# Kernel optimization log

Measured on AMD Instinct MI355X. Metric: run time of the kernel, lower is better.

Reference implementation:

```python
import jax, jax.numpy as jnp
import numpy as np

D, L, C, CP, H, HD, QB, KB = 8, 2048, 128, 16, 4, 32, 32, 128
NQ = L // QB

def _ln(x, eps=1e-5):
    m = jnp.mean(x, axis=-1, keepdims=True)
    v = jnp.var(x, axis=-1, keepdims=True)
    return (x - m) * jax.lax.rsqrt(v + eps)

def _ada_ln(a, s, Wg, bg, Ws):
    # AF3 AdaLN: gated layernorm conditioned on s
    an = _ln(a); sn = _ln(s)
    return jax.nn.sigmoid(sn @ Wg + bg) * an + sn @ Ws

def setup_inputs() -> dict:
    key = jax.random.key(0)
    ks = jax.random.split(key, 32)
    p = lambda i, shape: jax.random.normal(ks[i], shape, dtype=jnp.float32) * 0.02
    inp = {}
    inp['A_I'] = jax.random.normal(ks[0], (D, L, C), dtype=jnp.float32)
    inp['S_I'] = jax.random.normal(ks[1], (D, L, C), dtype=jnp.float32)
    inp['Z_II'] = jax.random.normal(ks[2], (1, L, L, CP), dtype=jnp.float32)
    # static sliding-window indices: 128-key window centered on each 32-query block
    inp['indicesQ'] = jnp.arange(L, dtype=jnp.int64).reshape(NQ, QB)
    kraw = (jnp.arange(NQ) * QB - (KB - QB) // 2)[:, None] + jnp.arange(KB)[None, :]
    inp['indicesK'] = jnp.clip(kraw, 0, L - 1).astype(jnp.int64)
    inp['maskQ_float'] = jnp.zeros((NQ, QB), jnp.float32)
    inp['maskK_float'] = ((kraw < 0) | (kraw >= L)).astype(jnp.float32)
    # parameters
    inp['ada1_Wg'] = p(3, (C, C)); inp['ada1_bg'] = jnp.zeros((C,), jnp.float32); inp['ada1_Ws'] = p(4, (C, C))
    inp['Wq'] = p(5, (C, H * HD)); inp['bq'] = jnp.zeros((H * HD,), jnp.float32)
    inp['Wk'] = p(6, (C, H * HD)); inp['Wv'] = p(7, (C, H * HD))
    inp['ln0_g'] = jnp.ones((CP,), jnp.float32); inp['ln0_b'] = jnp.zeros((CP,), jnp.float32)
    inp['Wb'] = p(8, (CP, H))
    inp['Wg_attn'] = p(9, (C, H * HD))
    inp['Wa'] = p(10, (H * HD, C))
    inp['Wop'] = p(11, (C, C)); inp['bop'] = jnp.full((C,), -2.0, jnp.float32)
    inp['ada2_Wg'] = p(12, (C, C)); inp['ada2_bg'] = jnp.zeros((C,), jnp.float32); inp['ada2_Ws'] = p(13, (C, C))
    inp['W_sw'] = p(14, (C, 2 * C)); inp['W_lin'] = p(15, (C, 2 * C))
    inp['ct_Wg'] = p(16, (C, C)); inp['ct_bg'] = jnp.full((C,), -2.0, jnp.float32)
    inp['W_out2'] = p(17, (2 * C, C))
    return inp

def _forward(A_I, S_I, Z_II, indicesQ, indicesK, maskQ_float, maskK_float,
             ada1_Wg, ada1_bg, ada1_Ws, Wq, bq, Wk, Wv, ln0_g, ln0_b, Wb,
             Wg_attn, Wa, Wop, bop, ada2_Wg, ada2_bg, ada2_Ws, W_sw, W_lin,
             ct_Wg, ct_bg, W_out2):
    Dn, Lv = A_I.shape[0], A_I.shape[1]
    An = _ada_ln(A_I, S_I, ada1_Wg, ada1_bg, ada1_Ws)
    Q = (An @ Wq + bq).reshape(Dn, Lv, H, HD)
    K = (An @ Wk).reshape(Dn, Lv, H, HD)
    V = (An @ Wv).reshape(Dn, Lv, H, HD)
    B = ((_ln(Z_II) * ln0_g + ln0_b) @ Wb)[0]        # [L, L, H]
    G = jax.nn.sigmoid(An @ Wg_attn).reshape(Dn, Lv, H, HD)
    qs = Q[:, indicesQ]                              # [D, nq, qb, H, hd]
    ksub = K[:, indicesK]                            # [D, nq, kb, H, hd]
    vs = V[:, indicesK]
    attn = jnp.einsum('dnihc,dnjhc->dnijh', qs, ksub) / jnp.sqrt(jnp.float32(HD))
    bias = B[indicesQ[:, :, None], indicesK[:, None, :]]  # [nq, qb, kb, H]
    attn = attn + bias[None]
    mask = maskQ_float[None, :, :, None, None] + maskK_float[None, :, None, :, None]
    attn = attn - 1e9 * mask
    attn = jax.nn.softmax(attn, axis=-2)             # softmax over key window (j)
    af = jnp.einsum('dnijh,dnjhc->dnihc', attn, vs)
    af = af * (1.0 - maskQ_float)[None, :, :, None, None]
    af = af.reshape(Dn, -1, H, HD)[:, :Lv]
    af = (G * af).reshape(Dn, Lv, H * HD) @ Wa
    B_I = jax.nn.sigmoid(S_I @ Wop + bop) * af
    A = A_I + B_I
    an2 = _ada_ln(A, S_I, ada2_Wg, ada2_bg, ada2_Ws)
    b = jax.nn.silu(an2 @ W_sw) * (an2 @ W_lin)      # SwiGLU transition
    A = A + jax.nn.sigmoid(S_I @ ct_Wg + ct_bg) * (b @ W_out2)
    return A

def reference(A_I, S_I, Z_II, indicesQ, indicesK, maskQ_float, maskK_float,
              ada1_Wg, ada1_bg, ada1_Ws, Wq, bq, Wk, Wv, ln0_g, ln0_b, Wb,
              Wg_attn, Wa, Wop, bop, ada2_Wg, ada2_bg, ada2_Ws, W_sw, W_lin,
              ct_Wg, ct_bg, W_out2):
    return _forward(A_I, S_I, Z_II, indicesQ, indicesK, maskQ_float, maskK_float,
                    ada1_Wg, ada1_bg, ada1_Ws, Wq, bq, Wk, Wv, ln0_g, ln0_b, Wb,
                    Wg_attn, Wa, Wop, bop, ada2_Wg, ada2_bg, ada2_Ws, W_sw, W_lin,
                    ct_Wg, ct_bg, W_out2)
```

## Files before the change

### kernel.cpp

```cpp
#include <hip/hip_runtime.h>

#define DL 16384
#define LL 2048
#define NQB 64
#define QBS 32
#define KBS 128

typedef __attribute__((ext_vector_type(8))) short short8;
typedef __attribute__((ext_vector_type(4))) short short4v;
typedef __attribute__((ext_vector_type(4))) float f32x4;

__device__ __forceinline__ float sigmoidf_(float x) { return 1.f / (1.f + expf(-x)); }

__device__ __forceinline__ short f2bf(float f) {
    union { float f; unsigned u; } v; v.f = f;
    unsigned r = (v.u + 0x7FFFu + ((v.u >> 16) & 1u)) >> 16;
    return (short)r;
}
__device__ __forceinline__ float bf2f(short h) {
    union { unsigned u; float f; } v; v.u = ((unsigned)(unsigned short)h) << 16;
    return v.f;
}

#define AFRAG(buf, stride, r0, kk) (*(const short8*)&(buf)[(size_t)((r0) + cl) * (stride) + (kk) * 32 + kg * 8])
#define WFRAG(Wt, K, n0, kk) (*(const short8*)((Wt) + (size_t)((n0) + cl) * (K) + (kk) * 32 + kg * 8))
#define MFMA(acc, a, b) acc = __builtin_amdgcn_mfma_f32_16x16x32_bf16(a, b, acc, 0, 0, 0)

__global__ __launch_bounds__(256) void k_prep(
    const float* __restrict__ W0, const float* __restrict__ W1, const float* __restrict__ W2,
    const float* __restrict__ W3, const float* __restrict__ W4, const float* __restrict__ W5,
    const float* __restrict__ W6, const float* __restrict__ W7, const float* __restrict__ W8,
    const float* __restrict__ W9, const float* __restrict__ W10,
    const float* __restrict__ Wsw, const float* __restrict__ Wlin, const float* __restrict__ Wout2,
    const float* __restrict__ Z, const float* __restrict__ g16, const float* __restrict__ b16,
    const float* __restrict__ Wb,
    short* __restrict__ wout, short* __restrict__ BBt)
{
    __shared__ float sW[128 * 128];
    __shared__ float sWb[64], sg[16], sb[16];
    __shared__ short sT[4 * 4 * 128];
    const int b = blockIdx.x;
    const int tid = threadIdx.x;

    if (b < 17) {
        const float* srcs[14] = {W0,W1,W2,W3,W4,W5,W6,W7,W8,W9,W10,Wsw,Wlin,Wout2};
        const int sel[17]  = {0,1,2,3,4,5,6,7,8,9,10,11,11,12,12,13,13};
        const int soff[17] = {0,0,0,0,0,0,0,0,0,0,0, 0,128, 0,128, 0,16384};
        const int sN[17]   = {128,128,128,128,128,128,128,128,128,128,128, 256,256,256,256, 128,128};
        const int doff[17] = {0,16384,32768,49152,65536,81920,98304,114688,131072,147456,163840,
                              180224,196608, 212992,229376, 245760,245888};
        const int dK[17]   = {128,128,128,128,128,128,128,128,128,128,128, 128,128,128,128, 256,256};
        const float* src = srcs[sel[b]] + soff[b];
        const int srcN = sN[b];
        short* dst = wout + doff[b];
        const int dstK = dK[b];
        {
            const int r = tid >> 1, ch = (tid & 1) * 64;
            #pragma unroll
            for (int u = 0; u < 16; ++u) {
                float4 v = *(const float4*)(src + (size_t)r * srcN + ch + u * 4);
                *(float4*)&sW[r * 128 + ch + u * 4] = v;
            }
        }
        __syncthreads();
        {
            const int o = tid >> 1, kh = (tid & 1) * 64;
            #pragma unroll
            for (int u8 = 0; u8 < 8; ++u8) {
                short8 pk;
                #pragma unroll
                for (int e = 0; e < 8; ++e)
                    pk[e] = f2bf(sW[(kh + u8 * 8 + e) * 128 + o]);
                *(short8*)(dst + (size_t)o * dstK + kh + u8 * 8) = pk;
            }
        }
    } else {
        const int bb = b - 17;
        const int n = bb >> 3;
        const int io = (bb & 7) * 4;
        if (tid < 64) sWb[tid] = Wb[tid];
        if (tid < 16) { sg[tid] = g16[tid]; sb[tid] = b16[tid]; }
        __syncthreads();
        #pragma unroll
        for (int p = 0; p < 2; ++p) {
            int pair = tid + 256 * p;
            int il = pair >> 7, j = pair & 127;
            int i = io + il;
            int kr = n * 32 - 48 + j;
            int kc = min(max(kr, 0), LL - 1);
            const float4* z4 = (const float4*)(Z + ((long)(n * 32 + i) * LL + kc) * 16);
            float zv[16];
            #pragma unroll
            for (int w = 0; w < 4; ++w) {
                float4 v = z4[w];
                zv[w * 4 + 0] = v.x; zv[w * 4 + 1] = v.y; zv[w * 4 + 2] = v.z; zv[w * 4 + 3] = v.w;
            }
            float sm = 0.f, sq = 0.f;
            #pragma unroll
            for (int cp = 0; cp < 16; ++cp) { sm += zv[cp]; sq = fmaf(zv[cp], zv[cp], sq); }
            float m = sm * (1.f / 16.f);
            float rs = rsqrtf(sq * (1.f / 16.f) - m * m + 1e-5f);
            float b0 = 0.f, b1 = 0.f, b2 = 0.f, b3 = 0.f;
            #pragma unroll
            for (int cp = 0; cp < 16; ++cp) {
                float zn = (zv[cp] - m) * rs * sg[cp] + sb[cp];
                b0 = fmaf(zn, sWb[cp * 4 + 0], b0);
                b1 = fmaf(zn, sWb[cp * 4 + 1], b1);
                b2 = fmaf(zn, sWb[cp * 4 + 2], b2);
                b3 = fmaf(zn, sWb[cp * 4 + 3], b3);
            }
            sT[(0 * 4 + il) * 128 + j] = f2bf(b0);
            sT[(1 * 4 + il) * 128 + j] = f2bf(b1);
            sT[(2 * 4 + il) * 128 + j] = f2bf(b2);
            sT[(3 * 4 + il) * 128 + j] = f2bf(b3);
        }
        __syncthreads();
        #pragma unroll
        for (int rr = 0; rr < 2; ++rr) {
            int cid = tid + rr * 256;
            int hh = cid >> 7, j = cid & 127;
            short4v pk;
            #pragma unroll
            for (int e = 0; e < 4; ++e) pk[e] = sT[(hh * 4 + e) * 128 + j];
            *(short4v*)(BBt + (((size_t)n * 4 + hh) * 128 + j) * 32 + io) = pk;
        }
    }
}

__global__ __launch_bounds__(512) void k_adaln_qkvg(
    const float* __restrict__ A_I, const float* __restrict__ S_I,
    const short* __restrict__ Wg1t, const short* __restrict__ Ws1t,
    const short* __restrict__ Wqt, const short* __restrict__ Wkt,
    const short* __restrict__ Wvt, const short* __restrict__ Wgat,
    const float* __restrict__ bg1, const float* __restrict__ bq,
    short* __restrict__ Qo, short* __restrict__ Ko, short* __restrict__ Vo, short* __restrict__ Go)
{
    __shared__ short sAr[32 * 136];
    __shared__ short sSn[32 * 136];
    __shared__ short sAn[32 * 136];
    __shared__ float sMean[32], sRstd[32];
    const int tid = threadIdx.x;
    const int lane = tid & 63;
    const long t0 = (long)blockIdx.x * 32;

    {
        const int row = tid >> 4, seg = tid & 15;
        const float* ap = A_I + (t0 + row) * 128 + seg * 8;
        const float* sp = S_I + (t0 + row) * 128 + seg * 8;
        float av[8], sv[8];
        #pragma unroll
        for (int u = 0; u < 2; ++u) {
            float4 a4 = ((const float4*)ap)[u];
            float4 s4 = ((const float4*)sp)[u];
            av[4*u] = a4.x; av[4*u+1] = a4.y; av[4*u+2] = a4.z; av[4*u+3] = a4.w;
            sv[4*u] = s4.x; sv[4*u+1] = s4.y; sv[4*u+2] = s4.z; sv[4*u+3] = s4.w;
        }
        float am = 0.f, aq = 0.f, sm = 0.f, sq = 0.f;
        #pragma unroll
        for (int u = 0; u < 8; ++u) {
            am += av[u]; aq = fmaf(av[u], av[u], aq);
            sm += sv[u]; sq = fmaf(sv[u], sv[u], sq);
        }
        am += __shfl_xor(am, 1); am += __shfl_xor(am, 2); am += __shfl_xor(am, 4); am += __shfl_xor(am, 8);
        aq += __shfl_xor(aq, 1); aq += __shfl_xor(aq, 2); aq += __shfl_xor(aq, 4); aq += __shfl_xor(aq, 8);
        sm += __shfl_xor(sm, 1); sm += __shfl_xor(sm, 2); sm += __shfl_xor(sm, 4); sm += __shfl_xor(sm, 8);
        sq += __shfl_xor(sq, 1); sq += __shfl_xor(sq, 2); sq += __shfl_xor(sq, 4); sq += __shfl_xor(sq, 8);
        float amean = am * (1.f / 128.f);
        float arstd = rsqrtf(aq * (1.f / 128.f) - amean * amean + 1e-5f);
        float smean = sm * (1.f / 128.f);
        float srstd = rsqrtf(sq * (1.f / 128.f) - smean * smean + 1e-5f);
        if ((tid & 15) == 0) { sMean[row] = amean; sRstd[row] = arstd; }
        short8 pa, ps;
        #pragma unroll
        for (int e = 0; e < 8; ++e) {
            pa[e] = f2bf(av[e]);
            ps[e] = f2bf((sv[e] - smean) * srstd);
        }
        *(short8*)&sAr[row * 136 + seg * 8] = pa;
        *(short8*)&sSn[row * 136 + seg * 8] = ps;
    }
    __syncthreads();
    const int w = tid >> 6;
    const int n0 = w * 16;
    const int cl = lane & 15, kg = lane >> 4;
    {
        short8 wg[4], wsf[4];
        #pragma unroll
        for (int kk = 0; kk < 4; ++kk) {
            wg[kk]  = WFRAG(Wg1t, 128, n0, kk);
            wsf[kk] = WFRAG(Ws1t, 128, n0, kk);
        }
        #pragma unroll
        for (int mt = 0; mt < 2; ++mt) {
            f32x4 ag = {0.f, 0.f, 0.f, 0.f}, as = {0.f, 0.f, 0.f, 0.f};
            #pragma unroll
            for (int kk = 0; kk < 4; ++kk) {
                short8 a = AFRAG(sSn, 136, mt * 16, kk);
                MFMA(ag, a, wg[kk]);
                MFMA(as, a, wsf[kk]);
            }
            const int col = n0 + cl;
            float bgc = bg1[col];
            #pragma unroll
            for (int i = 0; i < 4; ++i) {
                int r = mt * 16 + kg * 4 + i;
                float an = (bf2f(sAr[r * 136 + col]) - sMean[r]) * sRstd[r];
                float An = sigmoidf_(ag[i] + bgc) * an + as[i];
                sAn[r * 136 + col] = f2bf(An);
            }
        }
    }
    __syncthreads();
    {
        const float SCL = 0.17677669529663687f;
        short8 af[2][4];
        #pragma unroll
        for (int mt = 0; mt < 2; ++mt)
            #pragma unroll
            for (int kk = 0; kk < 4; ++kk)
                af[mt][kk] = AFRAG(sAn, 136, mt * 16, kk);
        #pragma unroll
        for (int m = 0; m < 4; ++m) {
            const short* Wt = (m == 0) ? Wqt : (m == 1) ? Wkt : (m == 2) ? Wvt : Wgat;
            short8 wf[4];
            #pragma unroll
            for (int kk = 0; kk < 4; ++kk) wf[kk] = WFRAG(Wt, 128, n0, kk);
            #pragma unroll
            for (int mt = 0; mt < 2; ++mt) {
                f32x4 acc = {0.f, 0.f, 0.f, 0.f};
                #pragma unroll
                for (int kk = 0; kk < 4; ++kk) MFMA(acc, af[mt][kk], wf[kk]);
                const int col = n0 + cl;
                #pragma unroll
                for (int i = 0; i < 4; ++i) {
                    long t = t0 + mt * 16 + kg * 4 + i;
                    float v = acc[i];
                    if (m == 0)      Qo[t * 128 + col] = f2bf((v + bq[col]) * SCL);
                    else if (m == 1) Ko[t * 128 + col] = f2bf(v);
                    else if (m == 2) Vo[t * 128 + col] = f2bf(v);
                    else             Go[t * 128 + col] = f2bf(sigmoidf_(v));
                }
            }
        }
    }
}

__global__ __launch_bounds__(256) void k_attn(
    const short* __restrict__ Qg, const short* __restrict__ Kg, const short* __restrict__ Vg,
    const short* __restrict__ Gg, const short* __restrict__ BBt, const float* __restrict__ maskK,
    short* __restrict__ AFo)
{
    __shared__ short vts[4 * 32 * 136];
    __shared__ short Pl [4 * 32 * 136];
    const int n = blockIdx.x, d = blockIdx.y;
    const int tid = threadIdx.x;
    const int lane = tid & 63;
    const int h = tid >> 6;
    const long tb = (long)d * LL;
    const int kbase = n * 32 - 48;
    short* vtsH = vts + h * 4352;
    short* PH   = Pl  + h * 4352;
    const int cl = lane & 15, kg = lane >> 4;

    {
        const int j0 = lane * 2;
        int kc0 = min(max(kbase + j0, 0), LL - 1);
        int kc1 = min(max(kbase + j0 + 1, 0), LL - 1);
        const short8* p0 = (const short8*)(Vg + (tb + kc0) * 128 + h * 32);
        const short8* p1 = (const short8*)(Vg + (tb + kc1) * 128 + h * 32);
        short8 ev[4] = {p0[0], p0[1], p0[2], p0[3]};
        short8 ov[4] = {p1[0], p1[1], p1[2], p1[3]};
        #pragma unroll
        for (int g = 0; g < 4; ++g)
            #pragma unroll
            for (int e = 0; e < 8; ++e)
                *(unsigned*)&vtsH[(g * 8 + e) * 136 + j0] =
                    (unsigned)(unsigned short)ev[g][e] | ((unsigned)(unsigned short)ov[g][e] << 16);
    }
    __syncthreads();

    float sc[2][8][4];
    {
        short8 qf[2];
        #pragma unroll
        for (int mt = 0; mt < 2; ++mt)
            qf[mt] = *(const short8*)(Qg + (tb + n * 32 + mt * 16 + cl) * 128 + h * 32 + kg * 8);
        #pragma unroll
        for (int nt = 0; nt < 8; ++nt) {
            const int key = nt * 16 + cl;
            int kc = min(max(kbase + key, 0), LL - 1);
            short8 kf = *(const short8*)(Kg + (tb + kc) * 128 + h * 32 + kg * 8);
            float mk = maskK[n * 128 + key] * 1e9f;
            #pragma unroll
            for (int mt = 0; mt < 2; ++mt) {
                f32x4 s = {0.f, 0.f, 0.f, 0.f};
                MFMA(s, qf[mt], kf);
                short4v bfr = *(const short4v*)(BBt + (((size_t)n * 4 + h) * 128 + key) * 32 + mt * 16 + kg * 4);
                #pragma unroll
                for (int i = 0; i < 4; ++i)
                    sc[mt][nt][i] = s[i] + bf2f(bfr[i]) - mk;
            }
        }
    }
    {
        #pragma unroll
        for (int mt = 0; mt < 2; ++mt) {
            #pragma unroll
            for (int i = 0; i < 4; ++i) {
                float mx = sc[mt][0][i];
                #pragma unroll
                for (int nt = 1; nt < 8; ++nt) mx = fmaxf(mx, sc[mt][nt][i]);
                mx = fmaxf(mx, __shfl_xor(mx, 1));
                mx = fmaxf(mx, __shfl_xor(mx, 2));
                mx = fmaxf(mx, __shfl_xor(mx, 4));
                mx = fmaxf(mx, __shfl_xor(mx, 8));
                float sm = 0.f;
                #pragma unroll
                for (int nt = 0; nt < 8; ++nt) {
                    float p = __expf(sc[mt][nt][i] - mx);
                    sc[mt][nt][i] = p; sm += p;
                }
                sm += __shfl_xor(sm, 1);
                sm += __shfl_xor(sm, 2);
                sm += __shfl_xor(sm, 4);
                sm += __shfl_xor(sm, 8);
                float inv = 1.f / sm;
                const int q = mt * 16 + kg * 4 + i;
                #pragma unroll
                for (int nt = 0; nt < 8; ++nt)
                    PH[q * 136 + nt * 16 + cl] = f2bf(sc[mt][nt][i] * inv);
            }
        }
    }
    __syncthreads();
    {
        #pragma unroll
        for (int mt = 0; mt < 2; ++mt) {
            #pragma unroll
            for (int ct = 0; ct < 2; ++ct) {
                f32x4 acc = {0.f, 0.f, 0.f, 0.f};
                #pragma unroll
                for (int kk = 0; kk < 4; ++kk) {
                    short8 a = *(const short8*)&PH[(mt * 16 + cl) * 136 + kk * 32 + kg * 8];
                    short8 b = *(const short8*)&vtsH[(ct * 16 + cl) * 136 + kk * 32 + kg * 8];
                    MFMA(acc, a, b);
                }
                const int col = h * 32 + ct * 16 + cl;
                #pragma unroll
                for (int i = 0; i < 4; ++i) {
                    long t = tb + n * 32 + mt * 16 + kg * 4 + i;
                    float g = bf2f(Gg[t * 128 + col]);
                    AFo[t * 128 + col] = f2bf(g * acc[i]);
                }
            }
        }
    }
}

__global__ __launch_bounds__(512) void k_postf(
    const short* __restrict__ AF, const float* __restrict__ S_I, const float* __restrict__ A_I,
    const short* __restrict__ Wat, const short* __restrict__ Wopt, const short* __restrict__ ctWgt,
    const short* __restrict__ Wg2t, const short* __restrict__ Ws2t,
    const short* __restrict__ Wswt, const short* __restrict__ Wlint, const short* __restrict__ Wout2t,
    const float* __restrict__ bop, const float* __restrict__ ctbg, const float* __restrict__ bg2,
    float* __restrict__ Out)
{
    __shared__ __align__(16) char smem[43264];
    short* sAF  = (short*)smem;
    short* sS   = (short*)(smem + 8704);
    short* sSn  = (short*)(smem + 17408);
    float* sA   = (float*)(smem + 26112);
    float* sMean = (float*)(smem + 43008);
    float* sRstd = (float*)(smem + 43136);
    short* sAn2 = sAF;
    short* sB   = (short*)(smem + 8704);

    const int tid = threadIdx.x;
    const int lane = tid & 63;
    const long t0 = (long)blockIdx.x * 32;

    {
        const int row = tid >> 4, seg = tid & 15;
        *(short8*)&sAF[row * 136 + seg * 8] =
            *(const short8*)(AF + (t0 + row) * 128 + seg * 8);
        const float* apI = A_I + (t0 + row) * 128 + seg * 8;
        #pragma unroll
        for (int u = 0; u < 2; ++u)
            *(float4*)&sA[row * 132 + seg * 8 + u * 4] = ((const float4*)apI)[u];
        const float* sp = S_I + (t0 + row) * 128 + seg * 8;
        float sv[8];
        #pragma unroll
        for (int u = 0; u < 2; ++u) {
            float4 s4 = ((const float4*)sp)[u];
            sv[4*u] = s4.x; sv[4*u+1] = s4.y; sv[4*u+2] = s4.z; sv[4*u+3] = s4.w;
        }
        float sm = 0.f, sq = 0.f;
        #pragma unroll
        for (int u = 0; u < 8; ++u) { sm += sv[u]; sq = fmaf(sv[u], sv[u], sq); }
        sm += __shfl_xor(sm, 1); sm += __shfl_xor(sm, 2); sm += __shfl_xor(sm, 4); sm += __shfl_xor(sm, 8);
        sq += __shfl_xor(sq, 1); sq += __shfl_xor(sq, 2); sq += __shfl_xor(sq, 4); sq += __shfl_xor(sq, 8);
        float smean = sm * (1.f / 128.f);
        float srstd = rsqrtf(sq * (1.f / 128.f) - smean * smean + 1e-5f);
        short8 pr, pn;
        #pragma unroll
        for (int e = 0; e < 8; ++e) {
            float s = sv[e];
            pr[e] = f2bf(s);
            pn[e] = f2bf((s - smean) * srstd);
        }
        *(short8*)&sS [row * 136 + seg * 8] = pr;
        *(short8*)&sSn[row * 136 + seg * 8] = pn;
    }
    __syncthreads();
    const int w = tid >> 6;
    const int n0 = w * 16;
    const int cl = lane & 15, kg = lane >> 4;
    float g2s[8];

    {
        short8 wA[4], wO[4], wG[4];
        #pragma unroll
        for (int kk = 0; kk < 4; ++kk) {
            wA[kk] = WFRAG(Wat, 128, n0, kk);
            wO[kk] = WFRAG(Wopt, 128, n0, kk);
            wG[kk] = WFRAG(ctWgt, 128, n0, kk);
        }
        #pragma unroll
        for (int mt = 0; mt < 2; ++mt) {
            f32x4 aA = {0.f,0.f,0.f,0.f}, aO = {0.f,0.f,0.f,0.f}, aG = {0.f,0.f,0.f,0.f};
            #pragma unroll
            for (int kk = 0; kk < 4; ++kk) {
                short8 af = AFRAG(sAF, 136, mt * 16, kk);
                short8 sf = AFRAG(sS, 136, mt * 16, kk);
                MFMA(aA, af, wA[kk]);
                MFMA(aO, sf, wO[kk]);
                MFMA(aG, sf, wG[kk]);
            }
            const int col = n0 + cl;
            float bopc = bop[col], ctc = ctbg[col];
            #pragma unroll
            for (int i = 0; i < 4; ++i) {
                int r = mt * 16 + kg * 4 + i;
                float Aval = sA[r * 132 + col] + sigmoidf_(aO[i] + bopc) * aA[i];
                sA[r * 132 + col] = Aval;
                g2s[mt * 4 + i] = sigmoidf_(aG[i] + ctc);
            }
        }
    }
    __syncthreads();
    {
        const int row = tid >> 4, seg = tid & 15;
        float m = 0.f, q = 0.f;
        #pragma unroll
        for (int u = 0; u < 2; ++u) {
            float4 v = *(const float4*)&sA[row * 132 + seg * 8 + u * 4];
            m += v.x + v.y + v.z + v.w;
            q = fmaf(v.x, v.x, q); q = fmaf(v.y, v.y, q);
            q = fmaf(v.z, v.z, q); q = fmaf(v.w, v.w, q);
        }
        m += __shfl_xor(m, 1); m += __shfl_xor(m, 2); m += __shfl_xor(m, 4); m += __shfl_xor(m, 8);
        q += __shfl_xor(q, 1); q += __shfl_xor(q, 2); q += __shfl_xor(q, 4); q += __shfl_xor(q, 8);
        float mean = m * (1.f / 128.f);
        float rstd = rsqrtf(q * (1.f / 128.f) - mean * mean + 1e-5f);
        if ((tid & 15) == 0) { sMean[row] = mean; sRstd[row] = rstd; }
    }
    __syncthreads();
    {
        short8 wg2[4], ws2[4];
        #pragma unroll
        for (int kk = 0; kk < 4; ++kk) {
            wg2[kk] = WFRAG(Wg2t, 128, n0, kk);
            ws2[kk] = WFRAG(Ws2t, 128, n0, kk);
        }
        #pragma unroll
        for (int mt = 0; mt < 2; ++mt) {
            f32x4 ag = {0.f,0.f,0.f,0.f}, as = {0.f,0.f,0.f,0.f};
            #pragma unroll
            for (int kk = 0; kk < 4; ++kk) {
                short8 a = AFRAG(sSn, 136, mt * 16, kk);
                MFMA(ag, a, wg2[kk]);
                MFMA(as, a, ws2[kk]);
            }
            const int col = n0 + cl;
            float bg2c = bg2[col];
            #pragma unroll
            for (int i = 0; i < 4; ++i) {
                int r = mt * 16 + kg * 4 + i;
                float lnA = (sA[r * 132 + col] - sMean[r]) * sRstd[r];
                sAn2[r * 136 + col] = f2bf(sigmoidf_(ag[i] + bg2c) * lnA + as[i]);
            }
        }
    }
    __syncthreads();
    {
        short8 a2f[2][4];
        #pragma unroll
        for (int mt = 0; mt < 2; ++mt)
            #pragma unroll
            for (int kk = 0; kk < 4; ++kk)
                a2f[mt][kk] = AFRAG(sAn2, 136, mt * 16, kk);
        #pragma unroll
        for (int j = 0; j < 2; ++j) {
            const int n0b = w * 32 + j * 16;
            short8 ww[4], wl[4];
            #pragma unroll
            for (int kk = 0; kk < 4; ++kk) {
                ww[kk] = WFRAG(Wswt, 128, n0b, kk);
                wl[kk] = WFRAG(Wlint, 128, n0b, kk);
            }
            #pragma unroll
            for (int mt = 0; mt < 2; ++mt) {
                f32x4 aw = {0.f,0.f,0.f,0.f}, al = {0.f,0.f,0.f,0.f};
                #pragma unroll
                for (int kk = 0; kk < 4; ++kk) {
                    MFMA(aw, a2f[mt][kk], ww[kk]);
                    MFMA(al, a2f[mt][kk], wl[kk]);
                }
                const int col2 = n0b + cl;
                #pragma unroll
                for (int i = 0; i < 4; ++i) {
                    int r = mt * 16 + kg * 4 + i;
                    float x = aw[i];
                    float bb = (x / (1.f + expf(-x))) * al[i];
                    sB[r * 264 + col2] = f2bf(bb);
                }
            }
        }
    }
    __syncthreads();
    {
        short8 wo[8];
        #pragma unroll
        for (int kk = 0; kk < 8; ++kk) wo[kk] = WFRAG(Wout2t, 256, n0, kk);
        #pragma unroll
        for (int mt = 0; mt < 2; ++mt) {
            f32x4 acc = {0.f,0.f,0.f,0.f};
            #pragma unroll
            for (int kk = 0; kk < 8; ++kk) {
                short8 a = AFRAG(sB, 264, mt * 16, kk);
                MFMA(acc, a, wo[kk]);
            }
            const int col = n0 + cl;
            #pragma unroll
            for (int i = 0; i < 4; ++i) {
                int r = mt * 16 + kg * 4 + i;
                long t = t0 + r;
                Out[t * 128 + col] = sA[r * 132 + col] + g2s[mt * 4 + i] * acc[i];
            }
        }
    }
}

extern "C" void kernel_launch(void* const* d_in, const int* in_sizes, int n_in,
                              void* d_out, int out_size, void* d_ws, size_t ws_size,
                              hipStream_t stream)
{
    const float* A_I  = (const float*)d_in[0];
    const float* S_I  = (const float*)d_in[1];
    const float* Z    = (const float*)d_in[2];
    const float* maskK = (const float*)d_in[6];
    const float* a1Wg = (const float*)d_in[7];
    const float* a1bg = (const float*)d_in[8];
    const float* a1Ws = (const float*)d_in[9];
    const float* Wq   = (const float*)d_in[10];
    const float* bq   = (const float*)d_in[11];
    const float* Wk   = (const float*)d_in[12];
    const float* Wv   = (const float*)d_in[13];
    const float* ln0g = (const float*)d_in[14];
    const float* ln0b = (const float*)d_in[15];
    const float* Wb   = (const float*)d_in[16];
    const float* Wga  = (const float*)d_in[17];
    const float* Wa   = (const float*)d_in[18];
    const float* Wop  = (const float*)d_in[19];
    const float* bop  = (const float*)d_in[20];
    const float* a2Wg = (const float*)d_in[21];
    const float* a2bg = (const float*)d_in[22];
    const float* a2Ws = (const float*)d_in[23];
    const float* Wsw  = (const float*)d_in[24];
    const float* Wlin = (const float*)d_in[25];
    const float* ctWg = (const float*)d_in[26];
    const float* ctbg = (const float*)d_in[27];
    const float* Wout2 = (const float*)d_in[28];
    float* out = (float*)d_out;

    const size_t NTC = (size_t)DL * 128;
    short* Qb = (short*)d_ws;
    short* Kb = Qb + NTC;
    short* Vb = Kb + NTC;
    short* Gb = Vb + NTC;
    short* BBt = Gb + NTC;
    short* wbt = BBt + (size_t)NQB * 4 * 128 * 32;
    short* AFb = Qb;

    short* Wg1t = wbt + 0 * 16384;
    short* Ws1t = wbt + 1 * 16384;
    short* Wqt  = wbt + 2 * 16384;
    short* Wkt  = wbt + 3 * 16384;
    short* Wvt  = wbt + 4 * 16384;
    short* Wgat = wbt + 5 * 16384;
    short* Wat  = wbt + 6 * 16384;
    short* Wopt = wbt + 7 * 16384;
    short* ctWgt = wbt + 8 * 16384;
    short* Wg2t = wbt + 9 * 16384;
    short* Ws2t = wbt + 10 * 16384;
    short* Wswt = wbt + 180224;
    short* Wlint = wbt + 212992;
    short* Wout2t = wbt + 245760;

    k_prep<<<529, 256, 0, stream>>>(a1Wg, a1Ws, Wq, Wk, Wv, Wga, Wa, Wop, ctWg,
                                    a2Wg, a2Ws, Wsw, Wlin, Wout2,
                                    Z, ln0g, ln0b, Wb, wbt, BBt);
    k_adaln_qkvg<<<DL / 32, 512, 0, stream>>>(A_I, S_I, Wg1t, Ws1t, Wqt, Wkt, Wvt, Wgat,
                                              a1bg, bq, Qb, Kb, Vb, Gb);
    k_attn<<<dim3(NQB, 8), 256, 0, stream>>>(Qb, Kb, Vb, Gb, BBt, maskK, AFb);
    k_postf<<<DL / 32, 512, 0, stream>>>(AFb, S_I, A_I, Wat, Wopt, ctWgt, Wg2t, Ws2t,
                                         Wswt, Wlint, Wout2t, bop, ctbg, a2bg, out);
}
```

Measured before the change: 76.00 us.

## Keep softmax probabilities in registers and split attention query tiles across blocks

New measurement: 82.00 us. 1.08x slower.

```diff
diff --git a/kernel.cpp b/kernel.cpp
--- a/kernel.cpp
+++ b/kernel.cpp
@@ -17,9 +17,16 @@
     unsigned r = (v.u + 0x7FFFu + ((v.u >> 16) & 1u)) >> 16;
     return (short)r;
 }
+__device__ __forceinline__ unsigned f2bfu(float f) {
+    union { float f; unsigned u; } v; v.f = f;
+    return (v.u + 0x7FFFu + ((v.u >> 16) & 1u)) >> 16;
+}
 __device__ __forceinline__ float bf2f(short h) {
     union { unsigned u; float f; } v; v.u = ((unsigned)(unsigned short)h) << 16;
     return v.f;
+}
+__device__ __forceinline__ unsigned packbf(float a, float b) {
+    return (f2bfu(a) & 0xFFFFu) | (f2bfu(b) << 16);
 }
 
 #define AFRAG(buf, stride, r0, kk) (*(const short8*)&(buf)[(size_t)((r0) + cl) * (stride) + (kk) * 32 + kg * 8])
@@ -81,48 +88,52 @@
         if (tid < 64) sWb[tid] = Wb[tid];
         if (tid < 16) { sg[tid] = g16[tid]; sb[tid] = b16[tid]; }
         __syncthreads();
-        #pragma unroll
-        for (int p = 0; p < 2; ++p) {
-            int pair = tid + 256 * p;
-            int il = pair >> 7, j = pair & 127;
+        const int q4 = tid & 3;
+        #pragma unroll
+        for (int p = 0; p < 8; ++p) {
+            int pairIdx = p * 64 + (tid >> 2);
+            int il = pairIdx >> 7, j = pairIdx & 127;
             int i = io + il;
             int kr = n * 32 - 48 + j;
             int kc = min(max(kr, 0), LL - 1);
-            const float4* z4 = (const float4*)(Z + ((long)(n * 32 + i) * LL + kc) * 16);
-            float zv[16];
-            #pragma unroll
-            for (int w = 0; w < 4; ++w) {
-                float4 v = z4[w];
-                zv[w * 4 + 0] = v.x; zv[w * 4 + 1] = v.y; zv[w * 4 + 2] = v.z; zv[w * 4 + 3] = v.w;
-            }
-            float sm = 0.f, sq = 0.f;
-            #pragma unroll
-            for (int cp = 0; cp < 16; ++cp) { sm += zv[cp]; sq = fmaf(zv[cp], zv[cp], sq); }
+            float4 zv = *(const float4*)(Z + ((long)(n * 32 + i) * LL + kc) * 16 + q4 * 4);
+            float sm = zv.x + zv.y + zv.z + zv.w;
+            float sq = fmaf(zv.x, zv.x, fmaf(zv.y, zv.y, fmaf(zv.z, zv.z, zv.w * zv.w)));
+            sm += __shfl_xor(sm, 1); sm += __shfl_xor(sm, 2);
+            sq += __shfl_xor(sq, 1); sq += __shfl_xor(sq, 2);
             float m = sm * (1.f / 16.f);
             float rs = rsqrtf(sq * (1.f / 16.f) - m * m + 1e-5f);
+            float zn[4];
+            zn[0] = (zv.x - m) * rs * sg[q4 * 4 + 0] + sb[q4 * 4 + 0];
+            zn[1] = (zv.y - m) * rs * sg[q4 * 4 + 1] + sb[q4 * 4 + 1];
+            zn[2] = (zv.z - m) * rs * sg[q4 * 4 + 2] + sb[q4 * 4 + 2];
+            zn[3] = (zv.w - m) * rs * sg[q4 * 4 + 3] + sb[q4 * 4 + 3];
             float b0 = 0.f, b1 = 0.f, b2 = 0.f, b3 = 0.f;
             #pragma unroll
-            for (int cp = 0; cp < 16; ++cp) {
-                float zn = (zv[cp] - m) * rs * sg[cp] + sb[cp];
-                b0 = fmaf(zn, sWb[cp * 4 + 0], b0);
-                b1 = fmaf(zn, sWb[cp * 4 + 1], b1);
-                b2 = fmaf(zn, sWb[cp * 4 + 2], b2);
-                b3 = fmaf(zn, sWb[cp * 4 + 3], b3);
-            }
-            sT[(0 * 4 + il) * 128 + j] = f2bf(b0);
-            sT[(1 * 4 + il) * 128 + j] = f2bf(b1);
-            sT[(2 * 4 + il) * 128 + j] = f2bf(b2);
-            sT[(3 * 4 + il) * 128 + j] = f2bf(b3);
+            for (int e = 0; e < 4; ++e) {
+                int cp = q4 * 4 + e;
+                b0 = fmaf(zn[e], sWb[cp * 4 + 0], b0);
+                b1 = fmaf(zn[e], sWb[cp * 4 + 1], b1);
+                b2 = fmaf(zn[e], sWb[cp * 4 + 2], b2);
+                b3 = fmaf(zn[e], sWb[cp * 4 + 3], b3);
+            }
+            b0 += __shfl_xor(b0, 1); b0 += __shfl_xor(b0, 2);
+            b1 += __shfl_xor(b1, 1); b1 += __shfl_xor(b1, 2);
+            b2 += __shfl_xor(b2, 1); b2 += __shfl_xor(b2, 2);
+            b3 += __shfl_xor(b3, 1); b3 += __shfl_xor(b3, 2);
+            float vh = (q4 == 0) ? b0 : (q4 == 1) ? b1 : (q4 == 2) ? b2 : b3;
+            sT[(q4 * 4 + il) * 128 + j] = f2bf(vh);
         }
         __syncthreads();
         #pragma unroll
         for (int rr = 0; rr < 2; ++rr) {
             int cid = tid + rr * 256;
-            int hh = cid >> 7, j = cid & 127;
+            int hh = cid >> 7, r2 = cid & 127;
+            int il = r2 >> 5, jb = (r2 & 31) * 4;
             short4v pk;
             #pragma unroll
-            for (int e = 0; e < 4; ++e) pk[e] = sT[(hh * 4 + e) * 128 + j];
-            *(short4v*)(BBt + (((size_t)n * 4 + hh) * 128 + j) * 32 + io) = pk;
+            for (int e = 0; e < 4; ++e) pk[e] = sT[(hh * 4 + il) * 128 + jb + e];
+            *(short4v*)(BBt + (((size_t)n * 4 + hh) * 32 + io + il) * 128 + jb) = pk;
         }
     }
 }
@@ -251,15 +262,13 @@
     short* __restrict__ AFo)
 {
     __shared__ short vts[4 * 32 * 136];
-    __shared__ short Pl [4 * 32 * 136];
-    const int n = blockIdx.x, d = blockIdx.y;
+    const int n = blockIdx.x, d = blockIdx.y, mt = blockIdx.z;
     const int tid = threadIdx.x;
     const int lane = tid & 63;
     const int h = tid >> 6;
     const long tb = (long)d * LL;
     const int kbase = n * 32 - 48;
     short* vtsH = vts + h * 4352;
-    short* PH   = Pl  + h * 4352;
     const int cl = lane & 15, kg = lane >> 4;
 
     {
@@ -277,82 +286,83 @@
                 *(unsigned*)&vtsH[(g * 8 + e) * 136 + j0] =
                     (unsigned)(unsigned short)ev[g][e] | ((unsigned)(unsigned short)ov[g][e] << 16);
     }
-    __syncthreads();
-
-    float sc[2][8][4];
-    {
-        short8 qf[2];
-        #pragma unroll
-        for (int mt = 0; mt < 2; ++mt)
-            qf[mt] = *(const short8*)(Qg + (tb + n * 32 + mt * 16 + cl) * 128 + h * 32 + kg * 8);
+
+    float sc[8][4];
+    {
+        short8 qf = *(const short8*)(Qg + (tb + n * 32 + mt * 16 + cl) * 128 + h * 32 + kg * 8);
         #pragma unroll
         for (int nt = 0; nt < 8; ++nt) {
-            const int key = nt * 16 + cl;
-            int kc = min(max(kbase + key, 0), LL - 1);
+            int kc = min(max(kbase + nt * 16 + cl, 0), LL - 1);
             short8 kf = *(const short8*)(Kg + (tb + kc) * 128 + h * 32 + kg * 8);
-            float mk = maskK[n * 128 + key] * 1e9f;
-            #pragma unroll
-            for (int mt = 0; mt < 2; ++mt) {
-                f32x4 s = {0.f, 0.f, 0.f, 0.f};
-                MFMA(s, qf[mt], kf);
-                short4v bfr = *(const short4v*)(BBt + (((size_t)n * 4 + h) * 128 + key) * 32 + mt * 16 + kg * 4);
-                #pragma unroll
-                for (int i = 0; i < 4; ++i)
-                    sc[mt][nt][i] = s[i] + bf2f(bfr[i]) - mk;
-            }
-        }
-    }
-    {
-        #pragma unroll
-        for (int mt = 0; mt < 2; ++mt) {
+            f32x4 s = {0.f, 0.f, 0.f, 0.f};
+            MFMA(s, kf, qf);
+            float4 mk4 = *(const float4*)(maskK + n * 128 + nt * 16 + kg * 4);
+            short4v bfr = *(const short4v*)(BBt + (((size_t)n * 4 + h) * 32 + mt * 16 + cl) * 128 + nt * 16 + kg * 4);
+            #pragma unroll
+            for (int i = 0; i < 4; ++i)
+                sc[nt][i] = s[i] + bf2f(bfr[i]) - mk4[i] * 1e9f;
+        }
+    }
+    unsigned bfrag[4][4];
+    {
+        float mx = sc[0][0];
+        #pragma unroll
+        for (int nt = 0; nt < 8; ++nt)
+            #pragma unroll
+            for (int i = 0; i < 4; ++i) mx = fmaxf(mx, sc[nt][i]);
+        mx = fmaxf(mx, __shfl_xor(mx, 16));
+        mx = fmaxf(mx, __shfl_xor(mx, 32));
+        float sm = 0.f;
+        #pragma unroll
+        for (int nt = 0; nt < 8; ++nt)
             #pragma unroll
             for (int i = 0; i < 4; ++i) {
-                float mx = sc[mt][0][i];
-                #pragma unroll
-                for (int nt = 1; nt < 8; ++nt) mx = fmaxf(mx, sc[mt][nt][i]);
-                mx = fmaxf(mx, __shfl_xor(mx, 1));
-                mx = fmaxf(mx, __shfl_xor(mx, 2));
-                mx = fmaxf(mx, __shfl_xor(mx, 4));
-                mx = fmaxf(mx, __shfl_xor(mx, 8));
-                float sm = 0.f;
-                #pragma unroll
-                for (int nt = 0; nt < 8; ++nt) {
-                    float p = __expf(sc[mt][nt][i] - mx);
-                    sc[mt][nt][i] = p; sm += p;
-                }
-                sm += __shfl_xor(sm, 1);
-                sm += __shfl_xor(sm, 2);
-                sm += __shfl_xor(sm, 4);
-                sm += __shfl_xor(sm, 8);
-                float inv = 1.f / sm;
-                const int q = mt * 16 + kg * 4 + i;
-                #pragma unroll
-                for (int nt = 0; nt < 8; ++nt)
-                    PH[q * 136 + nt * 16 + cl] = f2bf(sc[mt][nt][i] * inv);
-            }
-        }
-    }
-    __syncthreads();
-    {
-        #pragma unroll
-        for (int mt = 0; mt < 2; ++mt) {
-            #pragma unroll
-            for (int ct = 0; ct < 2; ++ct) {
-                f32x4 acc = {0.f, 0.f, 0.f, 0.f};
-                #pragma unroll
-                for (int kk = 0; kk < 4; ++kk) {
-                    short8 a = *(const short8*)&PH[(mt * 16 + cl) * 136 + kk * 32 + kg * 8];
-                    short8 b = *(const short8*)&vtsH[(ct * 16 + cl) * 136 + kk * 32 + kg * 8];
-                    MFMA(acc, a, b);
-                }
-                const int col = h * 32 + ct * 16 + cl;
-                #pragma unroll
-                for (int i = 0; i < 4; ++i) {
-                    long t = tb + n * 32 + mt * 16 + kg * 4 + i;
-                    float g = bf2f(Gg[t * 128 + col]);
-                    AFo[t * 128 + col] = f2bf(g * acc[i]);
-                }
-            }
+                float p = __expf(sc[nt][i] - mx);
+                sc[nt][i] = p; sm += p;
+            }
+        sm += __shfl_xor(sm, 16);
+        sm += __shfl_xor(sm, 32);
+        float inv = 1.f / sm;
+        #pragma unroll
+        for (int c2 = 0; c2 < 4; ++c2) {
+            unsigned E0 = packbf(sc[2*c2][0] * inv, sc[2*c2][1] * inv);
+            unsigned E1 = packbf(sc[2*c2][2] * inv, sc[2*c2][3] * inv);
+            unsigned O0 = packbf(sc[2*c2+1][0] * inv, sc[2*c2+1][1] * inv);
+            unsigned O1 = packbf(sc[2*c2+1][2] * inv, sc[2*c2+1][3] * inv);
+            unsigned t0 = (kg < 2) ? O0 : E0;
+            unsigned t1 = (kg < 2) ? O1 : E1;
+            unsigned r10 = __shfl_xor((int)t0, 32);
+            unsigned r11 = __shfl_xor((int)t1, 32);
+            unsigned u0 = (kg == 0 || kg == 3) ? r10 : (kg == 1 ? E0 : O0);
+            unsigned u1 = (kg == 0 || kg == 3) ? r11 : (kg == 1 ? E1 : O1);
+            unsigned r20 = __shfl_xor((int)u0, 16);
+            unsigned r21 = __shfl_xor((int)u1, 16);
+            bfrag[c2][0] = (kg == 0) ? E0 : (kg == 2) ? r10 : r20;
+            bfrag[c2][1] = (kg == 0) ? E1 : (kg == 2) ? r11 : r21;
+            bfrag[c2][2] = (kg == 0) ? r20 : (kg == 1) ? r10 : (kg == 2) ? r20 : O0;
+            bfrag[c2][3] = (kg == 0) ? r21 : (kg == 1) ? r11 : (kg == 2) ? r21 : O1;
+        }
+    }
+    __syncthreads();
+    {
+        #pragma unroll
+        for (int ct = 0; ct < 2; ++ct) {
+            f32x4 acc = {0.f, 0.f, 0.f, 0.f};
+            #pragma unroll
+            for (int c2 = 0; c2 < 4; ++c2) {
+                short8 a = *(const short8*)&vtsH[(ct * 16 + cl) * 136 + c2 * 32 + kg * 8];
+                union { unsigned u[4]; short8 s; } bb;
+                bb.u[0] = bfrag[c2][0]; bb.u[1] = bfrag[c2][1];
+                bb.u[2] = bfrag[c2][2]; bb.u[3] = bfrag[c2][3];
+                MFMA(acc, a, bb.s);
+            }
+            long t = tb + n * 32 + mt * 16 + cl;
+            const int c0 = h * 32 + ct * 16 + kg * 4;
+            short4v g4 = *(const short4v*)(Gg + t * 128 + c0);
+            short4v o4;
+            #pragma unroll
+            for (int i = 0; i < 4; ++i) o4[i] = f2bf(bf2f(g4[i]) * acc[i]);
+            *(short4v*)(AFo + t * 128 + c0) = o4;
         }
     }
 }
@@ -589,7 +599,7 @@
     short* Vb = Kb + NTC;
     short* Gb = Vb + NTC;
     short* BBt = Gb + NTC;
-    short* wbt = BBt + (size_t)NQB * 4 * 128 * 32;
+    short* wbt = BBt + (size_t)NQB * 4 * 32 * 128;
     short* AFb = Qb;
 
     short* Wg1t = wbt + 0 * 16384;
@@ -612,7 +622,7 @@
                                     Z, ln0g, ln0b, Wb, wbt, BBt);
     k_adaln_qkvg<<<DL / 32, 512, 0, stream>>>(A_I, S_I, Wg1t, Ws1t, Wqt, Wkt, Wvt, Wgat,
                                               a1bg, bq, Qb, Kb, Vb, Gb);
-    k_attn<<<dim3(NQB, 8), 256, 0, stream>>>(Qb, Kb, Vb, Gb, BBt, maskK, AFb);
+    k_attn<<<dim3(NQB, 8, 2), 256, 0, stream>>>(Qb, Kb, Vb, Gb, BBt, maskK, AFb);
     k_postf<<<DL / 32, 512, 0, stream>>>(AFb, S_I, A_I, Wat, Wopt, ctWgt, Wg2t, Ws2t,
                                          Wswt, Wlint, Wout2t, bop, ctbg, a2bg, out);
 }
```

## Fuse windowed attention into post-attention FFN kernel, keep AF in shared memory

Applied to the files above, without the earlier changes.

Result: faster. 70.35 us (-7.4%).

```diff
diff --git a/kernel.cpp b/kernel.cpp
--- a/kernel.cpp
+++ b/kernel.cpp
@@ -17,9 +17,16 @@
     unsigned r = (v.u + 0x7FFFu + ((v.u >> 16) & 1u)) >> 16;
     return (short)r;
 }
+__device__ __forceinline__ unsigned f2bfu(float f) {
+    union { float f; unsigned u; } v; v.f = f;
+    return (v.u + 0x7FFFu + ((v.u >> 16) & 1u)) >> 16;
+}
 __device__ __forceinline__ float bf2f(short h) {
     union { unsigned u; float f; } v; v.u = ((unsigned)(unsigned short)h) << 16;
     return v.f;
+}
+__device__ __forceinline__ unsigned packbf16(short a, short b) {
+    return ((unsigned)(unsigned short)a) | (((unsigned)(unsigned short)b) << 16);
 }
 
 #define AFRAG(buf, stride, r0, kk) (*(const short8*)&(buf)[(size_t)((r0) + cl) * (stride) + (kk) * 32 + kg * 8])
@@ -245,128 +252,20 @@
     }
 }
 
-__global__ __launch_bounds__(256) void k_attn(
+__global__ __launch_bounds__(512) void k_attn_postf(
     const short* __restrict__ Qg, const short* __restrict__ Kg, const short* __restrict__ Vg,
     const short* __restrict__ Gg, const short* __restrict__ BBt, const float* __restrict__ maskK,
-    short* __restrict__ AFo)
-{
-    __shared__ short vts[4 * 32 * 136];
-    __shared__ short Pl [4 * 32 * 136];
-    const int n = blockIdx.x, d = blockIdx.y;
-    const int tid = threadIdx.x;
-    const int lane = tid & 63;
-    const int h = tid >> 6;
-    const long tb = (long)d * LL;
-    const int kbase = n * 32 - 48;
-    short* vtsH = vts + h * 4352;
-    short* PH   = Pl  + h * 4352;
-    const int cl = lane & 15, kg = lane >> 4;
-
-    {
-        const int j0 = lane * 2;
-        int kc0 = min(max(kbase + j0, 0), LL - 1);
-        int kc1 = min(max(kbase + j0 + 1, 0), LL - 1);
-        const short8* p0 = (const short8*)(Vg + (tb + kc0) * 128 + h * 32);
-        const short8* p1 = (const short8*)(Vg + (tb + kc1) * 128 + h * 32);
-        short8 ev[4] = {p0[0], p0[1], p0[2], p0[3]};
-        short8 ov[4] = {p1[0], p1[1], p1[2], p1[3]};
-        #pragma unroll
-        for (int g = 0; g < 4; ++g)
-            #pragma unroll
-            for (int e = 0; e < 8; ++e)
-                *(unsigned*)&vtsH[(g * 8 + e) * 136 + j0] =
-                    (unsigned)(unsigned short)ev[g][e] | ((unsigned)(unsigned short)ov[g][e] << 16);
-    }
-    __syncthreads();
-
-    float sc[2][8][4];
-    {
-        short8 qf[2];
-        #pragma unroll
-        for (int mt = 0; mt < 2; ++mt)
-            qf[mt] = *(const short8*)(Qg + (tb + n * 32 + mt * 16 + cl) * 128 + h * 32 + kg * 8);
-        #pragma unroll
-        for (int nt = 0; nt < 8; ++nt) {
-            const int key = nt * 16 + cl;
-            int kc = min(max(kbase + key, 0), LL - 1);
-            short8 kf = *(const short8*)(Kg + (tb + kc) * 128 + h * 32 + kg * 8);
-            float mk = maskK[n * 128 + key] * 1e9f;
-            #pragma unroll
-            for (int mt = 0; mt < 2; ++mt) {
-                f32x4 s = {0.f, 0.f, 0.f, 0.f};
-                MFMA(s, qf[mt], kf);
-                short4v bfr = *(const short4v*)(BBt + (((size_t)n * 4 + h) * 128 + key) * 32 + mt * 16 + kg * 4);
-                #pragma unroll
-                for (int i = 0; i < 4; ++i)
-                    sc[mt][nt][i] = s[i] + bf2f(bfr[i]) - mk;
-            }
-        }
-    }
-    {
-        #pragma unroll
-        for (int mt = 0; mt < 2; ++mt) {
-            #pragma unroll
-            for (int i = 0; i < 4; ++i) {
-                float mx = sc[mt][0][i];
-                #pragma unroll
-                for (int nt = 1; nt < 8; ++nt) mx = fmaxf(mx, sc[mt][nt][i]);
-                mx = fmaxf(mx, __shfl_xor(mx, 1));
-                mx = fmaxf(mx, __shfl_xor(mx, 2));
-                mx = fmaxf(mx, __shfl_xor(mx, 4));
-                mx = fmaxf(mx, __shfl_xor(mx, 8));
-                float sm = 0.f;
-                #pragma unroll
-                for (int nt = 0; nt < 8; ++nt) {
-                    float p = __expf(sc[mt][nt][i] - mx);
-                    sc[mt][nt][i] = p; sm += p;
-                }
-                sm += __shfl_xor(sm, 1);
-                sm += __shfl_xor(sm, 2);
-                sm += __shfl_xor(sm, 4);
-                sm += __shfl_xor(sm, 8);
-                float inv = 1.f / sm;
-                const int q = mt * 16 + kg * 4 + i;
-                #pragma unroll
-                for (int nt = 0; nt < 8; ++nt)
-                    PH[q * 136 + nt * 16 + cl] = f2bf(sc[mt][nt][i] * inv);
-            }
-        }
-    }
-    __syncthreads();
-    {
-        #pragma unroll
-        for (int mt = 0; mt < 2; ++mt) {
-            #pragma unroll
-            for (int ct = 0; ct < 2; ++ct) {
-                f32x4 acc = {0.f, 0.f, 0.f, 0.f};
-                #pragma unroll
-                for (int kk = 0; kk < 4; ++kk) {
-                    short8 a = *(const short8*)&PH[(mt * 16 + cl) * 136 + kk * 32 + kg * 8];
-                    short8 b = *(const short8*)&vtsH[(ct * 16 + cl) * 136 + kk * 32 + kg * 8];
-                    MFMA(acc, a, b);
-                }
-                const int col = h * 32 + ct * 16 + cl;
-                #pragma unroll
-                for (int i = 0; i < 4; ++i) {
-                    long t = tb + n * 32 + mt * 16 + kg * 4 + i;
-                    float g = bf2f(Gg[t * 128 + col]);
-                    AFo[t * 128 + col] = f2bf(g * acc[i]);
-                }
-            }
-        }
-    }
-}
-
-__global__ __launch_bounds__(512) void k_postf(
-    const short* __restrict__ AF, const float* __restrict__ S_I, const float* __restrict__ A_I,
+    const float* __restrict__ S_I, const float* __restrict__ A_I,
     const short* __restrict__ Wat, const short* __restrict__ Wopt, const short* __restrict__ ctWgt,
     const short* __restrict__ Wg2t, const short* __restrict__ Ws2t,
     const short* __restrict__ Wswt, const short* __restrict__ Wlint, const short* __restrict__ Wout2t,
     const float* __restrict__ bop, const float* __restrict__ ctbg, const float* __restrict__ bg2,
     float* __restrict__ Out)
 {
-    __shared__ __align__(16) char smem[43264];
+    __shared__ __align__(16) char smem[78336];
     short* sAF  = (short*)smem;
+    short* vts  = (short*)(smem + 8704);
+    short* Pl   = (short*)(smem + 43520);
     short* sS   = (short*)(smem + 8704);
     short* sSn  = (short*)(smem + 17408);
     float* sA   = (float*)(smem + 26112);
@@ -375,14 +274,105 @@
     short* sAn2 = sAF;
     short* sB   = (short*)(smem + 8704);
 
+    const int n = blockIdx.x, d = blockIdx.y;
     const int tid = threadIdx.x;
     const int lane = tid & 63;
-    const long t0 = (long)blockIdx.x * 32;
+    const long tb = (long)d * LL;
+    const long t0 = tb + n * 32;
+    const int kbase = n * 32 - 48;
+    const int cl = lane & 15, kg = lane >> 4;
+    const int w = tid >> 6;
+    const int h = w >> 1, amt = w & 1;
+
+    {
+        const int unit = tid >> 1, half = tid & 1;
+        const int hh = unit >> 6, j0 = (unit & 63) * 2;
+        int kc0 = min(max(kbase + j0, 0), LL - 1);
+        int kc1 = min(max(kbase + j0 + 1, 0), LL - 1);
+        const short8* p0 = (const short8*)(Vg + (tb + kc0) * 128 + hh * 32 + half * 16);
+        const short8* p1 = (const short8*)(Vg + (tb + kc1) * 128 + hh * 32 + half * 16);
+        short8 e0 = p0[0], e1 = p0[1];
+        short8 o0 = p1[0], o1 = p1[1];
+        short* vh = vts + hh * 4352;
+        #pragma unroll
+        for (int e = 0; e < 8; ++e)
+            *(unsigned*)&vh[(half * 16 + e) * 136 + j0] = packbf16(e0[e], o0[e]);
+        #pragma unroll
+        for (int e = 0; e < 8; ++e)
+            *(unsigned*)&vh[(half * 16 + 8 + e) * 136 + j0] = packbf16(e1[e], o1[e]);
+    }
+
+    float sc[8][4];
+    {
+        short8 qf = *(const short8*)(Qg + (t0 + amt * 16 + cl) * 128 + h * 32 + kg * 8);
+        #pragma unroll
+        for (int nt = 0; nt < 8; ++nt) {
+            const int key = nt * 16 + cl;
+            int kc = min(max(kbase + key, 0), LL - 1);
+            short8 kf = *(const short8*)(Kg + (tb + kc) * 128 + h * 32 + kg * 8);
+            float mk = maskK[n * 128 + key] * 1e9f;
+            f32x4 s = {0.f, 0.f, 0.f, 0.f};
+            MFMA(s, qf, kf);
+            short4v bfr = *(const short4v*)(BBt + (((size_t)n * 4 + h) * 128 + key) * 32 + amt * 16 + kg * 4);
+            #pragma unroll
+            for (int i = 0; i < 4; ++i)
+                sc[nt][i] = s[i] + bf2f(bfr[i]) - mk;
+        }
+    }
+    {
+        short* PH = Pl + h * 4352;
+        #pragma unroll
+        for (int i = 0; i < 4; ++i) {
+            float mx = sc[0][i];
+            #pragma unroll
+            for (int nt = 1; nt < 8; ++nt) mx = fmaxf(mx, sc[nt][i]);
+            mx = fmaxf(mx, __shfl_xor(mx, 1));
+            mx = fmaxf(mx, __shfl_xor(mx, 2));
+            mx = fmaxf(mx, __shfl_xor(mx, 4));
+            mx = fmaxf(mx, __shfl_xor(mx, 8));
+            float sm = 0.f;
+            #pragma unroll
+            for (int nt = 0; nt < 8; ++nt) {
+                float p = __expf(sc[nt][i] - mx);
+                sc[nt][i] = p; sm += p;
+            }
+            sm += __shfl_xor(sm, 1);
+            sm += __shfl_xor(sm, 2);
+            sm += __shfl_xor(sm, 4);
+            sm += __shfl_xor(sm, 8);
+            float inv = 1.f / sm;
+            const int q = amt * 16 + kg * 4 + i;
+            #pragma unroll
+            for (int nt = 0; nt < 8; ++nt)
+                PH[q * 136 + nt * 16 + cl] = f2bf(sc[nt][i] * inv);
+        }
+    }
+    __syncthreads();
+    {
+        short* PH = Pl + h * 4352;
+        short* vh = vts + h * 4352;
+        #pragma unroll
+        for (int ct = 0; ct < 2; ++ct) {
+            f32x4 acc = {0.f, 0.f, 0.f, 0.f};
+            #pragma unroll
+            for (int kk = 0; kk < 4; ++kk) {
+                short8 a = *(const short8*)&PH[(amt * 16 + cl) * 136 + kk * 32 + kg * 8];
+                short8 b = *(const short8*)&vh[(ct * 16 + cl) * 136 + kk * 32 + kg * 8];
+                MFMA(acc, a, b);
+            }
+            const int col = h * 32 + ct * 16 + cl;
+            #pragma unroll
+            for (int i = 0; i < 4; ++i) {
+                int r = amt * 16 + kg * 4 + i;
+                float g = bf2f(Gg[(t0 + r) * 128 + col]);
+                sAF[r * 136 + col] = f2bf(g * acc[i]);
+            }
+        }
+    }
+    __syncthreads();
 
     {
         const int row = tid >> 4, seg = tid & 15;
-        *(short8*)&sAF[row * 136 + seg * 8] =
-            *(const short8*)(AF + (t0 + row) * 128 + seg * 8);
         const float* apI = A_I + (t0 + row) * 128 + seg * 8;
         #pragma unroll
         for (int u = 0; u < 2; ++u)
@@ -412,9 +402,7 @@
         *(short8*)&sSn[row * 136 + seg * 8] = pn;
     }
     __syncthreads();
-    const int w = tid >> 6;
     const int n0 = w * 16;
-    const int cl = lane & 15, kg = lane >> 4;
     float g2s[8];
 
     {
@@ -426,12 +414,12 @@
             wG[kk] = WFRAG(ctWgt, 128, n0, kk);
         }
         #pragma unroll
-        for (int mt = 0; mt < 2; ++mt) {
+        for (int rt = 0; rt < 2; ++rt) {
             f32x4 aA = {0.f,0.f,0.f,0.f}, aO = {0.f,0.f,0.f,0.f}, aG = {0.f,0.f,0.f,0.f};
             #pragma unroll
             for (int kk = 0; kk < 4; ++kk) {
-                short8 af = AFRAG(sAF, 136, mt * 16, kk);
-                short8 sf = AFRAG(sS, 136, mt * 16, kk);
+                short8 af = AFRAG(sAF, 136, rt * 16, kk);
+                short8 sf = AFRAG(sS, 136, rt * 16, kk);
                 MFMA(aA, af, wA[kk]);
                 MFMA(aO, sf, wO[kk]);
                 MFMA(aG, sf, wG[kk]);
@@ -440,10 +428,10 @@
             float bopc = bop[col], ctc = ctbg[col];
             #pragma unroll
             for (int i = 0; i < 4; ++i) {
-                int r = mt * 16 + kg * 4 + i;
+                int r = rt * 16 + kg * 4 + i;
                 float Aval = sA[r * 132 + col] + sigmoidf_(aO[i] + bopc) * aA[i];
                 sA[r * 132 + col] = Aval;
-                g2s[mt * 4 + i] = sigmoidf_(aG[i] + ctc);
+                g2s[rt * 4 + i] = sigmoidf_(aG[i] + ctc);
             }
         }
     }
@@ -473,11 +461,11 @@
             ws2[kk] = WFRAG(Ws2t, 128, n0, kk);
         }
         #pragma unroll
-        for (int mt = 0; mt < 2; ++mt) {
+        for (int rt = 0; rt < 2; ++rt) {
             f32x4 ag = {0.f,0.f,0.f,0.f}, as = {0.f,0.f,0.f,0.f};
             #pragma unroll
             for (int kk = 0; kk < 4; ++kk) {
-                short8 a = AFRAG(sSn, 136, mt * 16, kk);
+                short8 a = AFRAG(sSn, 136, rt * 16, kk);
                 MFMA(ag, a, wg2[kk]);
                 MFMA(as, a, ws2[kk]);
             }
@@ -485,7 +473,7 @@
             float bg2c = bg2[col];
             #pragma unroll
             for (int i = 0; i < 4; ++i) {
-                int r = mt * 16 + kg * 4 + i;
+                int r = rt * 16 + kg * 4 + i;
                 float lnA = (sA[r * 132 + col] - sMean[r]) * sRstd[r];
                 sAn2[r * 136 + col] = f2bf(sigmoidf_(ag[i] + bg2c) * lnA + as[i]);
             }
@@ -495,10 +483,10 @@
     {
         short8 a2f[2][4];
         #pragma unroll
-        for (int mt = 0; mt < 2; ++mt)
+        for (int rt = 0; rt < 2; ++rt)
             #pragma unroll
             for (int kk = 0; kk < 4; ++kk)
-                a2f[mt][kk] = AFRAG(sAn2, 136, mt * 16, kk);
+                a2f[rt][kk] = AFRAG(sAn2, 136, rt * 16, kk);
         #pragma unroll
         for (int j = 0; j < 2; ++j) {
             const int n0b = w * 32 + j * 16;
@@ -509,17 +497,17 @@
                 wl[kk] = WFRAG(Wlint, 128, n0b, kk);
             }
             #pragma unroll
-            for (int mt = 0; mt < 2; ++mt) {
+            for (int rt = 0; rt < 2; ++rt) {
                 f32x4 aw = {0.f,0.f,0.f,0.f}, al = {0.f,0.f,0.f,0.f};
                 #pragma unroll
                 for (int kk = 0; kk < 4; ++kk) {
-                    MFMA(aw, a2f[mt][kk], ww[kk]);
-                    MFMA(al, a2f[mt][kk], wl[kk]);
+                    MFMA(aw, a2f[rt][kk], ww[kk]);
+                    MFMA(al, a2f[rt][kk], wl[kk]);
                 }
                 const int col2 = n0b + cl;
                 #pragma unroll
                 for (int i = 0; i < 4; ++i) {
-                    int r = mt * 16 + kg * 4 + i;
+                    int r = rt * 16 + kg * 4 + i;
                     float x = aw[i];
                     float bb = (x / (1.f + expf(-x))) * al[i];
                     sB[r * 264 + col2] = f2bf(bb);
@@ -533,19 +521,19 @@
         #pragma unroll
         for (int kk = 0; kk < 8; ++kk) wo[kk] = WFRAG(Wout2t, 256, n0, kk);
         #pragma unroll
-        for (int mt = 0; mt < 2; ++mt) {
+        for (int rt = 0; rt < 2; ++rt) {
             f32x4 acc = {0.f,0.f,0.f,0.f};
             #pragma unroll
             for (int kk = 0; kk < 8; ++kk) {
-                short8 a = AFRAG(sB, 264, mt * 16, kk);
+                short8 a = AFRAG(sB, 264, rt * 16, kk);
                 MFMA(acc, a, wo[kk]);
             }
             const int col = n0 + cl;
             #pragma unroll
             for (int i = 0; i < 4; ++i) {
-                int r = mt * 16 + kg * 4 + i;
+                int r = rt * 16 + kg * 4 + i;
                 long t = t0 + r;
-                Out[t * 128 + col] = sA[r * 132 + col] + g2s[mt * 4 + i] * acc[i];
+                Out[t * 128 + col] = sA[r * 132 + col] + g2s[rt * 4 + i] * acc[i];
             }
         }
     }
@@ -590,7 +578,6 @@
     short* Gb = Vb + NTC;
     short* BBt = Gb + NTC;
     short* wbt = BBt + (size_t)NQB * 4 * 128 * 32;
-    short* AFb = Qb;
 
     short* Wg1t = wbt + 0 * 16384;
     short* Ws1t = wbt + 1 * 16384;
@@ -612,7 +599,9 @@
                                     Z, ln0g, ln0b, Wb, wbt, BBt);
     k_adaln_qkvg<<<DL / 32, 512, 0, stream>>>(A_I, S_I, Wg1t, Ws1t, Wqt, Wkt, Wvt, Wgat,
                                               a1bg, bq, Qb, Kb, Vb, Gb);
-    k_attn<<<dim3(NQB, 8), 256, 0, stream>>>(Qb, Kb, Vb, Gb, BBt, maskK, AFb);
-    k_postf<<<DL / 32, 512, 0, stream>>>(AFb, S_I, A_I, Wat, Wopt, ctWgt, Wg2t, Ws2t,
-                                         Wswt, Wlint, Wout2t, bop, ctbg, a2bg, out);
-}
+    k_attn_postf<<<dim3(NQB, 8), 512, 0, stream>>>(Qb, Kb, Vb, Gb, BBt, maskK,
+                                                   S_I, A_I,
+                                                   Wat, Wopt, ctWgt, Wg2t, Ws2t,
+                                                   Wswt, Wlint, Wout2t,
+                                                   bop, ctbg, a2bg, out);
+}
```
